# Performance work log

Hardware: AMD Instinct MI355X
Metric: run time of the kernel (lower is better)

Reference implementation:

```python
import jax, jax.numpy as jnp
import numpy as np

B, T, D, H, G = 256, 1024, 32, 64, 4 * 64  # batch, seq, input, hidden, gates


def setup_inputs() -> dict:
    key = jax.random.key(0)
    ks = jax.random.split(key, 12)
    s = 1.0 / np.sqrt(H)  # PyTorch LSTM default init scale
    return {
        "x": jax.random.normal(ks[0], (B, T, D), dtype=jnp.float32),
        "w_ih_l0": jax.random.normal(ks[1], (G, D), dtype=jnp.float32) * s,
        "w_hh_l0": jax.random.normal(ks[2], (G, H), dtype=jnp.float32) * s,
        "b_ih_l0": jax.random.normal(ks[3], (G,), dtype=jnp.float32) * s,
        "b_hh_l0": jax.random.normal(ks[4], (G,), dtype=jnp.float32) * s,
        "w_ih_l1": jax.random.normal(ks[5], (G, H), dtype=jnp.float32) * s,
        "w_hh_l1": jax.random.normal(ks[6], (G, H), dtype=jnp.float32) * s,
        "b_ih_l1": jax.random.normal(ks[7], (G,), dtype=jnp.float32) * s,
        "b_hh_l1": jax.random.normal(ks[8], (G,), dtype=jnp.float32) * s,
        "w_fc": jax.random.normal(ks[9], (1, H), dtype=jnp.float32) * s,
        "b_fc": jax.random.normal(ks[10], (1,), dtype=jnp.float32) * s,
    }


def _lstm_layer(x, w_ih, w_hh, b_ih, b_hh):
    """x: [B, T, Din] -> h_seq [B, T, H]. PyTorch gate order (i, f, g, o)."""
    # Precompute input contribution for all timesteps in one GEMM.
    gx = jnp.einsum('btd,gd->btg', x, w_ih) + b_ih + b_hh  # [B, T, 4H]
    gx = jnp.swapaxes(gx, 0, 1)  # [T, B, 4H] for scan over time
    h0 = jnp.zeros((x.shape[0], H), dtype=x.dtype)
    c0 = jnp.zeros((x.shape[0], H), dtype=x.dtype)

    def step(carry, g_t):
        h, c = carry
        g = g_t + h @ w_hh.T  # [B, 4H]
        i, f, gg, o = jnp.split(g, 4, axis=-1)
        i = jax.nn.sigmoid(i)
        f = jax.nn.sigmoid(f)
        gg = jnp.tanh(gg)
        o = jax.nn.sigmoid(o)
        c = f * c + i * gg
        h = o * jnp.tanh(c)
        return (h, c), h

    _, h_seq = jax.lax.scan(step, (h0, c0), gx)  # h_seq: [T, B, H]
    return jnp.swapaxes(h_seq, 0, 1)  # [B, T, H]


def reference(x, w_ih_l0, w_hh_l0, b_ih_l0, b_hh_l0,
              w_ih_l1, w_hh_l1, b_ih_l1, b_hh_l1, w_fc, b_fc):
    h1 = _lstm_layer(x, w_ih_l0, w_hh_l0, b_ih_l0, b_hh_l0)
    h2 = _lstm_layer(h1, w_ih_l1, w_hh_l1, b_ih_l1, b_hh_l1)
    last = h2[:, -1, :]  # [B, H]
    logits = last @ w_fc.T + b_fc  # [B, 1]
    return jax.nn.sigmoid(logits)
```

## Files before the change

### kernel.cpp

```cpp
#include <hip/hip_runtime.h>

#define TT 1024
#define DD 32
#define HH 64

typedef __fp16 h2v __attribute__((ext_vector_type(2)));
typedef _Float16 f16x8 __attribute__((ext_vector_type(8)));
typedef float f32x4 __attribute__((ext_vector_type(4)));

struct __attribute__((aligned(16))) H4 { h2v p[4]; };

__device__ __forceinline__ h2v pk(float a, float b) {
    return __builtin_amdgcn_cvt_pkrtz(a, b);
}
__device__ __forceinline__ float fsig(float x) {
    float e = __builtin_amdgcn_exp2f(-1.4426950408889634f * x);
    return __builtin_amdgcn_rcpf(1.0f + e);
}
__device__ __forceinline__ float ftanh(float x) {
    float e = __builtin_amdgcn_exp2f(2.885390081777927f * x);
    return 1.0f - 2.0f * __builtin_amdgcn_rcpf(1.0f + e);
}
__device__ __forceinline__ void bar_lds() {
    asm volatile("s_waitcnt lgkmcnt(0)\n\ts_barrier" ::: "memory");
}
__device__ __forceinline__ float pick4(f32x4 c, bool s0, bool s1) {
    float lo = s0 ? c[1] : c[0];
    float hi = s0 ? c[3] : c[2];
    return s1 ? hi : lo;
}
__device__ __forceinline__ f16x8 packx(float4 a, float4 b) {
    H4 t;
    t.p[0] = pk(a.x, a.y); t.p[1] = pk(a.z, a.w);
    t.p[2] = pk(b.x, b.y); t.p[3] = pk(b.z, b.w);
    return __builtin_bit_cast(f16x8, t);
}
__device__ __forceinline__ f16x8 load_afrag(const float* p) {
    return packx(*(const float4*)p, *(const float4*)(p + 4));
}
#define MFMA16(A, B, C) __builtin_amdgcn_mfma_f32_16x16x32_f16(A, B, C, 0, 0, 0)

__global__ __launch_bounds__(512) void lstm2_b4v2(
    const float* __restrict__ x,
    const float* __restrict__ w_ih_l0, const float* __restrict__ w_hh_l0,
    const float* __restrict__ b_ih_l0, const float* __restrict__ b_hh_l0,
    const float* __restrict__ w_ih_l1, const float* __restrict__ w_hh_l1,
    const float* __restrict__ b_ih_l1, const float* __restrict__ b_hh_l1,
    const float* __restrict__ w_fc,   const float* __restrict__ b_fc,
    float* __restrict__ out)
{
    const int bbase = blockIdx.x * 4;
    const int tid  = threadIdx.x;
    const int wave = tid >> 6;
    const int lane = tid & 63;
    const bool isL1 = wave < 4;
    const int js   = wave & 3;
    const int quad = lane >> 4;
    const int bb   = lane & 3;
    const int rsel = (lane >> 2) & 3;
    const int jj   = js*16 + quad*4 + rsel;
    const int mrow = lane & 15;

    __shared__ __attribute__((aligned(16))) __fp16 buf[1024];
    ((int*)buf)[tid] = 0;

    f16x8 A[16];
    float bs0, bs1, bs2, bs3;
    if (isL1) {
        #pragma unroll
        for (int q = 0; q < 4; ++q) {
            const int g = q*64 + js*16 + mrow;
            A[q*3 + 0] = load_afrag(w_ih_l0 + (size_t)g*DD + quad*8);
            A[q*3 + 1] = load_afrag(w_hh_l0 + (size_t)g*HH + quad*8);
            A[q*3 + 2] = load_afrag(w_hh_l0 + (size_t)g*HH + 32 + quad*8);
        }
        bs0 = b_ih_l0[0*64 + jj] + b_hh_l0[0*64 + jj];
        bs1 = b_ih_l0[1*64 + jj] + b_hh_l0[1*64 + jj];
        bs2 = b_ih_l0[2*64 + jj] + b_hh_l0[2*64 + jj];
        bs3 = b_ih_l0[3*64 + jj] + b_hh_l0[3*64 + jj];
    } else {
        #pragma unroll
        for (int q = 0; q < 4; ++q) {
            const int g = q*64 + js*16 + mrow;
            A[q*4 + 0] = load_afrag(w_ih_l1 + (size_t)g*HH + quad*8);
            A[q*4 + 1] = load_afrag(w_ih_l1 + (size_t)g*HH + 32 + quad*8);
            A[q*4 + 2] = load_afrag(w_hh_l1 + (size_t)g*HH + quad*8);
            A[q*4 + 3] = load_afrag(w_hh_l1 + (size_t)g*HH + 32 + quad*8);
        }
        bs0 = b_ih_l1[0*64 + jj] + b_hh_l1[0*64 + jj];
        bs1 = b_ih_l1[1*64 + jj] + b_hh_l1[1*64 + jj];
        bs2 = b_ih_l1[2*64 + jj] + b_hh_l1[2*64 + jj];
        bs3 = b_ih_l1[3*64 + jj] + b_hh_l1[3*64 + jj];
    }

    const int roff = (bb*4 + quad)*8;
    const int cw   = (isL1 ? 0 : 2) + (jj >> 5);
    const int woff = ((cw*4 + bb)*4 + ((jj & 31) >> 3))*8 + (jj & 7);

    const float* xg = x + (size_t)(bbase + bb) * (TT*DD) + quad*8;
    float4 r0a, r0b, r1a, r1b, r2a, r2b;
    if (isL1) {
        r0a = *(const float4*)(xg);          r0b = *(const float4*)(xg + 4);
        r1a = *(const float4*)(xg + DD);     r1b = *(const float4*)(xg + DD + 4);
        r2a = *(const float4*)(xg + 2*DD);   r2b = *(const float4*)(xg + 2*DD + 4);
    }

    __syncthreads();

    const bool s0 = (rsel & 1) != 0;
    const bool s1 = (rsel & 2) != 0;
    float cst = 0.0f;
    const f32x4 Z = {0.f, 0.f, 0.f, 0.f};

    for (int t = 0; t <= TT; ++t) {
        const int p = t & 1;
        const __fp16* bc = buf + p*512;
        __fp16* bn = buf + (p ^ 1)*512;
        if (isL1) {
            if (t < TT) {
                f16x8 Bx = packx(r0a, r0b);
                r0a = r1a; r0b = r1b; r1a = r2a; r1b = r2b;
                const int tl = (t + 3 < TT) ? (t + 3) : (TT - 1);
                r2a = *(const float4*)(xg + (size_t)tl*DD);
                r2b = *(const float4*)(xg + (size_t)tl*DD + 4);

                f16x8 B1 = *(const f16x8*)(bc + 0*128 + roff);
                f16x8 B2 = *(const f16x8*)(bc + 1*128 + roff);

                f32x4 C0 = MFMA16(A[0], Bx, Z);
                f32x4 C1 = MFMA16(A[3], Bx, Z);
                f32x4 C2 = MFMA16(A[6], Bx, Z);
                f32x4 C3 = MFMA16(A[9], Bx, Z);
                C0 = MFMA16(A[1],  B1, C0);
                C1 = MFMA16(A[4],  B1, C1);
                C2 = MFMA16(A[7],  B1, C2);
                C3 = MFMA16(A[10], B1, C3);
                f32x4 D0 = MFMA16(A[2],  B2, Z);
                f32x4 D1 = MFMA16(A[5],  B2, Z);
                f32x4 D2 = MFMA16(A[8],  B2, Z);
                f32x4 D3 = MFMA16(A[11], B2, Z);

                float Si = pick4(C0, s0, s1) + pick4(D0, s0, s1) + bs0;
                float Sf = pick4(C1, s0, s1) + pick4(D1, s0, s1) + bs1;
                float Sg = pick4(C2, s0, s1) + pick4(D2, s0, s1) + bs2;
                float So = pick4(C3, s0, s1) + pick4(D3, s0, s1) + bs3;

                float ii = fsig(Si), ff = fsig(Sf), oo = fsig(So);
                float gg = ftanh(Sg);
                cst = ff * cst + ii * gg;
                float hv = oo * ftanh(cst);
                bn[woff] = (__fp16)hv;
            }
        } else {
            if (t > 0) {
                f16x8 B1 = *(const f16x8*)(bc + 0*128 + roff);
                f16x8 B2 = *(const f16x8*)(bc + 1*128 + roff);
                f16x8 B3 = *(const f16x8*)(bc + 2*128 + roff);
                f16x8 B4 = *(const f16x8*)(bc + 3*128 + roff);

                f32x4 C0 = MFMA16(A[0],  B1, Z); C0 = MFMA16(A[1],  B2, C0);
                f32x4 C1 = MFMA16(A[4],  B1, Z); C1 = MFMA16(A[5],  B2, C1);
                f32x4 C2 = MFMA16(A[8],  B1, Z); C2 = MFMA16(A[9],  B2, C2);
                f32x4 C3 = MFMA16(A[12], B1, Z); C3 = MFMA16(A[13], B2, C3);
                f32x4 D0 = MFMA16(A[2],  B3, Z); D0 = MFMA16(A[3],  B4, D0);
                f32x4 D1 = MFMA16(A[6],  B3, Z); D1 = MFMA16(A[7],  B4, D1);
                f32x4 D2 = MFMA16(A[10], B3, Z); D2 = MFMA16(A[11], B4, D2);
                f32x4 D3 = MFMA16(A[14], B3, Z); D3 = MFMA16(A[15], B4, D3);

                float Si = pick4(C0, s0, s1) + pick4(D0, s0, s1) + bs0;
                float Sf = pick4(C1, s0, s1) + pick4(D1, s0, s1) + bs1;
                float Sg = pick4(C2, s0, s1) + pick4(D2, s0, s1) + bs2;
                float So = pick4(C3, s0, s1) + pick4(D3, s0, s1) + bs3;

                float ii = fsig(Si), ff = fsig(Sf), oo = fsig(So);
                float gg = ftanh(Sg);
                cst = ff * cst + ii * gg;
                float hv = oo * ftanh(cst);
                bn[woff] = (__fp16)hv;
            }
        }
        bar_lds();
    }

    if (wave == 0) {
        const int jg = lane >> 2;
        float s = 0.f;
        #pragma unroll
        for (int u2 = 0; u2 < 4; ++u2) {
            const int j = jg*4 + u2;
            float hval = (float)buf[512 + (((2 + (j >> 5))*4 + bb)*4 + ((j & 31) >> 3))*8 + (j & 7)];
            s += hval * w_fc[j];
        }
        s += __shfl_xor(s, 4);
        s += __shfl_xor(s, 8);
        s += __shfl_xor(s, 16);
        s += __shfl_xor(s, 32);
        if (lane < 4) out[bbase + lane] = fsig(s + b_fc[0]);
    }
}

extern "C" void kernel_launch(void* const* d_in, const int* in_sizes, int n_in,
                              void* d_out, int out_size, void* d_ws, size_t ws_size,
                              hipStream_t stream) {
    lstm2_b4v2<<<dim3(64), dim3(512), 0, stream>>>(
        (const float*)d_in[0],
        (const float*)d_in[1], (const float*)d_in[2],
        (const float*)d_in[3], (const float*)d_in[4],
        (const float*)d_in[5], (const float*)d_in[6],
        (const float*)d_in[7], (const float*)d_in[8],
        (const float*)d_in[9], (const float*)d_in[10],
        (float*)d_out);
}
```

Before: 666.7 us.

## Collapse each LSTM layer into one wave and sync every eight steps

The 8-wave block (4 waves per layer, with a barrier every timestep) becomes a 2-wave block. One wave computes all 64 hidden units of layer 0 and the other handles layer 1. The two layers are skewed by 8-step chunks through a 16-slot LDS ring, so a block barrier is needed only once per chunk. Within a layer the wave reads its own LDS writes, so there is no cross-wave sync inside a chunk. This removes most per-step barrier cost, but each wave now does four times the MFMA and transcendental work serially and holds 64 A fragments in registers, which increases register pressure and the per-step latency chain.

```diff
diff --git a/kernel.cpp b/kernel.cpp
--- a/kernel.cpp
+++ b/kernel.cpp
@@ -40,7 +40,7 @@
 }
 #define MFMA16(A, B, C) __builtin_amdgcn_mfma_f32_16x16x32_f16(A, B, C, 0, 0, 0)
 
-__global__ __launch_bounds__(512) void lstm2_b4v2(
+__global__ __launch_bounds__(128) void lstm2_wv(
     const float* __restrict__ x,
     const float* __restrict__ w_ih_l0, const float* __restrict__ w_hh_l0,
     const float* __restrict__ b_ih_l0, const float* __restrict__ b_hh_l0,
@@ -53,142 +53,161 @@
     const int tid  = threadIdx.x;
     const int wave = tid >> 6;
     const int lane = tid & 63;
-    const bool isL1 = wave < 4;
-    const int js   = wave & 3;
     const int quad = lane >> 4;
     const int bb   = lane & 3;
     const int rsel = (lane >> 2) & 3;
-    const int jj   = js*16 + quad*4 + rsel;
     const int mrow = lane & 15;
 
-    __shared__ __attribute__((aligned(16))) __fp16 buf[1024];
-    ((int*)buf)[tid] = 0;
-
-    f16x8 A[16];
-    float bs0, bs1, bs2, bs3;
-    if (isL1) {
-        #pragma unroll
-        for (int q = 0; q < 4; ++q) {
-            const int g = q*64 + js*16 + mrow;
-            A[q*3 + 0] = load_afrag(w_ih_l0 + (size_t)g*DD + quad*8);
-            A[q*3 + 1] = load_afrag(w_hh_l0 + (size_t)g*HH + quad*8);
-            A[q*3 + 2] = load_afrag(w_hh_l0 + (size_t)g*HH + 32 + quad*8);
-        }
-        bs0 = b_ih_l0[0*64 + jj] + b_hh_l0[0*64 + jj];
-        bs1 = b_ih_l0[1*64 + jj] + b_hh_l0[1*64 + jj];
-        bs2 = b_ih_l0[2*64 + jj] + b_hh_l0[2*64 + jj];
-        bs3 = b_ih_l0[3*64 + jj] + b_hh_l0[3*64 + jj];
+    __shared__ __attribute__((aligned(16))) __fp16 buf[4608];
+    {
+        int* bi = (int*)buf;
+        #pragma unroll
+        for (int i = 0; i < 18; ++i) bi[tid + i*128] = 0;
+    }
+
+    f16x8 A[64];
+    float bs[16];
+    int woffs[4];
+    if (wave == 0) {
+        #pragma unroll
+        for (int jg = 0; jg < 4; ++jg)
+            #pragma unroll
+            for (int q = 0; q < 4; ++q) {
+                const int g = q*64 + jg*16 + mrow;
+                A[jg*12 + q*3 + 0] = load_afrag(w_ih_l0 + (size_t)g*DD + quad*8);
+                A[jg*12 + q*3 + 1] = load_afrag(w_hh_l0 + (size_t)g*HH + quad*8);
+                A[jg*12 + q*3 + 2] = load_afrag(w_hh_l0 + (size_t)g*HH + 32 + quad*8);
+            }
+        #pragma unroll
+        for (int jg = 0; jg < 4; ++jg) {
+            const int jj = jg*16 + quad*4 + rsel;
+            #pragma unroll
+            for (int q = 0; q < 4; ++q)
+                bs[jg*4 + q] = b_ih_l0[q*64 + jj] + b_hh_l0[q*64 + jj];
+            woffs[jg] = (((jj >> 5)*4 + bb)*4 + ((jj & 31) >> 3))*8 + (jj & 7);
+        }
     } else {
         #pragma unroll
-        for (int q = 0; q < 4; ++q) {
-            const int g = q*64 + js*16 + mrow;
-            A[q*4 + 0] = load_afrag(w_ih_l1 + (size_t)g*HH + quad*8);
-            A[q*4 + 1] = load_afrag(w_ih_l1 + (size_t)g*HH + 32 + quad*8);
-            A[q*4 + 2] = load_afrag(w_hh_l1 + (size_t)g*HH + quad*8);
-            A[q*4 + 3] = load_afrag(w_hh_l1 + (size_t)g*HH + 32 + quad*8);
-        }
-        bs0 = b_ih_l1[0*64 + jj] + b_hh_l1[0*64 + jj];
-        bs1 = b_ih_l1[1*64 + jj] + b_hh_l1[1*64 + jj];
-        bs2 = b_ih_l1[2*64 + jj] + b_hh_l1[2*64 + jj];
-        bs3 = b_ih_l1[3*64 + jj] + b_hh_l1[3*64 + jj];
+        for (int jg = 0; jg < 4; ++jg)
+            #pragma unroll
+            for (int q = 0; q < 4; ++q) {
+                const int g = q*64 + jg*16 + mrow;
+                A[jg*16 + q*4 + 0] = load_afrag(w_ih_l1 + (size_t)g*HH + quad*8);
+                A[jg*16 + q*4 + 1] = load_afrag(w_ih_l1 + (size_t)g*HH + 32 + quad*8);
+                A[jg*16 + q*4 + 2] = load_afrag(w_hh_l1 + (size_t)g*HH + quad*8);
+                A[jg*16 + q*4 + 3] = load_afrag(w_hh_l1 + (size_t)g*HH + 32 + quad*8);
+            }
+        #pragma unroll
+        for (int jg = 0; jg < 4; ++jg) {
+            const int jj = jg*16 + quad*4 + rsel;
+            #pragma unroll
+            for (int q = 0; q < 4; ++q)
+                bs[jg*4 + q] = b_ih_l1[q*64 + jj] + b_hh_l1[q*64 + jj];
+            woffs[jg] = (((jj >> 5)*4 + bb)*4 + ((jj & 31) >> 3))*8 + (jj & 7);
+        }
     }
 
     const int roff = (bb*4 + quad)*8;
-    const int cw   = (isL1 ? 0 : 2) + (jj >> 5);
-    const int woff = ((cw*4 + bb)*4 + ((jj & 31) >> 3))*8 + (jj & 7);
 
     const float* xg = x + (size_t)(bbase + bb) * (TT*DD) + quad*8;
-    float4 r0a, r0b, r1a, r1b, r2a, r2b;
-    if (isL1) {
-        r0a = *(const float4*)(xg);          r0b = *(const float4*)(xg + 4);
-        r1a = *(const float4*)(xg + DD);     r1b = *(const float4*)(xg + DD + 4);
-        r2a = *(const float4*)(xg + 2*DD);   r2b = *(const float4*)(xg + 2*DD + 4);
+    f16x8 xr0 = {}, xr1 = {};
+    if (wave == 0) {
+        xr0 = packx(*(const float4*)xg, *(const float4*)(xg + 4));
+        xr1 = packx(*(const float4*)(xg + DD), *(const float4*)(xg + DD + 4));
     }
 
     __syncthreads();
 
     const bool s0 = (rsel & 1) != 0;
     const bool s1 = (rsel & 2) != 0;
-    float cst = 0.0f;
+    float cst[4] = {0.f, 0.f, 0.f, 0.f};
     const f32x4 Z = {0.f, 0.f, 0.f, 0.f};
 
-    for (int t = 0; t <= TT; ++t) {
-        const int p = t & 1;
-        const __fp16* bc = buf + p*512;
-        __fp16* bn = buf + (p ^ 1)*512;
-        if (isL1) {
-            if (t < TT) {
-                f16x8 Bx = packx(r0a, r0b);
-                r0a = r1a; r0b = r1b; r1a = r2a; r1b = r2b;
-                const int tl = (t + 3 < TT) ? (t + 3) : (TT - 1);
-                r2a = *(const float4*)(xg + (size_t)tl*DD);
-                r2b = *(const float4*)(xg + (size_t)tl*DD + 4);
-
-                f16x8 B1 = *(const f16x8*)(bc + 0*128 + roff);
-                f16x8 B2 = *(const f16x8*)(bc + 1*128 + roff);
-
-                f32x4 C0 = MFMA16(A[0], Bx, Z);
-                f32x4 C1 = MFMA16(A[3], Bx, Z);
-                f32x4 C2 = MFMA16(A[6], Bx, Z);
-                f32x4 C3 = MFMA16(A[9], Bx, Z);
-                C0 = MFMA16(A[1],  B1, C0);
-                C1 = MFMA16(A[4],  B1, C1);
-                C2 = MFMA16(A[7],  B1, C2);
-                C3 = MFMA16(A[10], B1, C3);
-                f32x4 D0 = MFMA16(A[2],  B2, Z);
-                f32x4 D1 = MFMA16(A[5],  B2, Z);
-                f32x4 D2 = MFMA16(A[8],  B2, Z);
-                f32x4 D3 = MFMA16(A[11], B2, Z);
-
-                float Si = pick4(C0, s0, s1) + pick4(D0, s0, s1) + bs0;
-                float Sf = pick4(C1, s0, s1) + pick4(D1, s0, s1) + bs1;
-                float Sg = pick4(C2, s0, s1) + pick4(D2, s0, s1) + bs2;
-                float So = pick4(C3, s0, s1) + pick4(D3, s0, s1) + bs3;
-
-                float ii = fsig(Si), ff = fsig(Sf), oo = fsig(So);
-                float gg = ftanh(Sg);
-                cst = ff * cst + ii * gg;
-                float hv = oo * ftanh(cst);
-                bn[woff] = (__fp16)hv;
+    for (int I = 0; I < 129; ++I) {
+        if (wave == 0) {
+            if (I < 128) {
+                for (int k = 0; k < 8; ++k) {
+                    const int t = I*8 + k;
+                    const __fp16* rs = buf + ((t + 15) & 15)*256;
+                    f16x8 B1 = *(const f16x8*)(rs + roff);
+                    f16x8 B2 = *(const f16x8*)(rs + 128 + roff);
+                    f16x8 Bx = xr0;
+                    xr0 = xr1;
+                    const int tn = (t + 2 < TT) ? (t + 2) : (TT - 1);
+                    xr1 = packx(*(const float4*)(xg + (size_t)tn*DD),
+                                *(const float4*)(xg + (size_t)tn*DD + 4));
+                    __fp16* ws = buf + (t & 15)*256;
+                    #pragma unroll
+                    for (int jg = 0; jg < 4; ++jg) {
+                        f32x4 C0 = MFMA16(A[jg*12+0], Bx, Z);
+                        f32x4 C1 = MFMA16(A[jg*12+3], Bx, Z);
+                        f32x4 C2 = MFMA16(A[jg*12+6], Bx, Z);
+                        f32x4 C3 = MFMA16(A[jg*12+9], Bx, Z);
+                        C0 = MFMA16(A[jg*12+1],  B1, C0); C0 = MFMA16(A[jg*12+2],  B2, C0);
+                        C1 = MFMA16(A[jg*12+4],  B1, C1); C1 = MFMA16(A[jg*12+5],  B2, C1);
+                        C2 = MFMA16(A[jg*12+7],  B1, C2); C2 = MFMA16(A[jg*12+8],  B2, C2);
+                        C3 = MFMA16(A[jg*12+10], B1, C3); C3 = MFMA16(A[jg*12+11], B2, C3);
+
+                        float Si = pick4(C0, s0, s1) + bs[jg*4+0];
+                        float Sf = pick4(C1, s0, s1) + bs[jg*4+1];
+                        float Sg = pick4(C2, s0, s1) + bs[jg*4+2];
+                        float So = pick4(C3, s0, s1) + bs[jg*4+3];
+
+                        float ii = fsig(Si), ff = fsig(Sf), oo = fsig(So);
+                        float gg = ftanh(Sg);
+                        cst[jg] = ff * cst[jg] + ii * gg;
+                        float hv = oo * ftanh(cst[jg]);
+                        ws[woffs[jg]] = (__fp16)hv;
+                    }
+                }
             }
         } else {
-            if (t > 0) {
-                f16x8 B1 = *(const f16x8*)(bc + 0*128 + roff);
-                f16x8 B2 = *(const f16x8*)(bc + 1*128 + roff);
-                f16x8 B3 = *(const f16x8*)(bc + 2*128 + roff);
-                f16x8 B4 = *(const f16x8*)(bc + 3*128 + roff);
-
-                f32x4 C0 = MFMA16(A[0],  B1, Z); C0 = MFMA16(A[1],  B2, C0);
-                f32x4 C1 = MFMA16(A[4],  B1, Z); C1 = MFMA16(A[5],  B2, C1);
-                f32x4 C2 = MFMA16(A[8],  B1, Z); C2 = MFMA16(A[9],  B2, C2);
-                f32x4 C3 = MFMA16(A[12], B1, Z); C3 = MFMA16(A[13], B2, C3);
-                f32x4 D0 = MFMA16(A[2],  B3, Z); D0 = MFMA16(A[3],  B4, D0);
-                f32x4 D1 = MFMA16(A[6],  B3, Z); D1 = MFMA16(A[7],  B4, D1);
-                f32x4 D2 = MFMA16(A[10], B3, Z); D2 = MFMA16(A[11], B4, D2);
-                f32x4 D3 = MFMA16(A[14], B3, Z); D3 = MFMA16(A[15], B4, D3);
-
-                float Si = pick4(C0, s0, s1) + pick4(D0, s0, s1) + bs0;
-                float Sf = pick4(C1, s0, s1) + pick4(D1, s0, s1) + bs1;
-                float Sg = pick4(C2, s0, s1) + pick4(D2, s0, s1) + bs2;
-                float So = pick4(C3, s0, s1) + pick4(D3, s0, s1) + bs3;
-
-                float ii = fsig(Si), ff = fsig(Sf), oo = fsig(So);
-                float gg = ftanh(Sg);
-                cst = ff * cst + ii * gg;
-                float hv = oo * ftanh(cst);
-                bn[woff] = (__fp16)hv;
+            if (I > 0) {
+                for (int k = 0; k < 8; ++k) {
+                    const int t = (I - 1)*8 + k;
+                    const __fp16* rs = buf + (t & 15)*256;
+                    f16x8 B1 = *(const f16x8*)(rs + roff);
+                    f16x8 B2 = *(const f16x8*)(rs + 128 + roff);
+                    const __fp16* h2r = buf + 4096 + (((t & 1) ^ 1))*256;
+                    f16x8 B3 = *(const f16x8*)(h2r + roff);
+                    f16x8 B4 = *(const f16x8*)(h2r + 128 + roff);
+                    __fp16* ws = buf + 4096 + (t & 1)*256;
+                    #pragma unroll
+                    for (int jg = 0; jg < 4; ++jg) {
+                        f32x4 C0 = MFMA16(A[jg*16+0],  B1, Z);
+                        f32x4 C1 = MFMA16(A[jg*16+4],  B1, Z);
+                        f32x4 C2 = MFMA16(A[jg*16+8],  B1, Z);
+                        f32x4 C3 = MFMA16(A[jg*16+12], B1, Z);
+                        C0 = MFMA16(A[jg*16+1],  B2, C0); C0 = MFMA16(A[jg*16+2],  B3, C0); C0 = MFMA16(A[jg*16+3],  B4, C0);
+                        C1 = MFMA16(A[jg*16+5],  B2, C1); C1 = MFMA16(A[jg*16+6],  B3, C1); C1 = MFMA16(A[jg*16+7],  B4, C1);
+                        C2 = MFMA16(A[jg*16+9],  B2, C2); C2 = MFMA16(A[jg*16+10], B3, C2); C2 = MFMA16(A[jg*16+11], B4, C2);
+                        C3 = MFMA16(A[jg*16+13], B2, C3); C3 = MFMA16(A[jg*16+14], B3, C3); C3 = MFMA16(A[jg*16+15], B4, C3);
+
+                        float Si = pick4(C0, s0, s1) + bs[jg*4+0];
+                        float Sf = pick4(C1, s0, s1) + bs[jg*4+1];
+                        float Sg = pick4(C2, s0, s1) + bs[jg*4+2];
+                        float So = pick4(C3, s0, s1) + bs[jg*4+3];
+
+                        float ii = fsig(Si), ff = fsig(Sf), oo = fsig(So);
+                        float gg = ftanh(Sg);
+                        cst[jg] = ff * cst[jg] + ii * gg;
+                        float hv = oo * ftanh(cst[jg]);
+                        ws[woffs[jg]] = (__fp16)hv;
+                    }
+                }
             }
         }
         bar_lds();
     }
 
-    if (wave == 0) {
-        const int jg = lane >> 2;
+    if (wave == 1) {
+        asm volatile("s_waitcnt lgkmcnt(0)" ::: "memory");
+        const int jg2 = lane >> 2;
         float s = 0.f;
         #pragma unroll
-        for (int u2 = 0; u2 < 4; ++u2) {
-            const int j = jg*4 + u2;
-            float hval = (float)buf[512 + (((2 + (j >> 5))*4 + bb)*4 + ((j & 31) >> 3))*8 + (j & 7)];
+        for (int u = 0; u < 4; ++u) {
+            const int j = jg2*4 + u;
+            float hval = (float)buf[4096 + 256 + (((j >> 5)*4 + bb)*4 + ((j & 31) >> 3))*8 + (j & 7)];
             s += hval * w_fc[j];
         }
         s += __shfl_xor(s, 4);
@@ -202,7 +221,7 @@
 extern "C" void kernel_launch(void* const* d_in, const int* in_sizes, int n_in,
                               void* d_out, int out_size, void* d_ws, size_t ws_size,
                               hipStream_t stream) {
-    lstm2_b4v2<<<dim3(64), dim3(512), 0, stream>>>(
+    lstm2_wv<<<dim3(64), dim3(128), 0, stream>>>(
         (const float*)d_in[0],
         (const float*)d_in[1], (const float*)d_in[2],
         (const float*)d_in[3], (const float*)d_in[4],
```

Result: slower. 1.742 ms (+161.3%).
